# Kernel optimization log

Measured on AMD Instinct MI355X. Metric: run time of the kernel, lower is better.

The kernel has to match this reference:

```python
import jax, jax.numpy as jnp
import numpy as np

K = 16                 # nn_k neighbors (self excluded)
FILTER_SCALE = 2.0
SHARPNESS_SIGMA = 0.75
EPS = 1e-17


def _eps_denom(x):
    return jnp.where(x < EPS, EPS, x)


def _normalize(x):
    # F.normalize(dim=-1) semantics
    return x / jnp.maximum(jnp.linalg.norm(x, axis=-1, keepdims=True), 1e-12)


def _gather(feat, idx):
    # feat: (B,P,D), idx: (B,P,K) -> (B,P,K,D)   (== pytorch3d knn_gather)
    return jnp.take_along_axis(feat[:, None, :, :], idx[:, :, :, None], axis=2)


def _knn(points, k):
    # points: (B,P,3) -> squared dists (B,P,k), idxs (B,P,k); self excluded
    d2 = jnp.sum(points * points, axis=-1)
    dists = d2[:, :, None] + d2[:, None, :] - 2.0 * jnp.einsum('bpd,bqd->bpq', points, points)
    P = points.shape[1]
    r = jnp.arange(P)
    dists = dists.at[:, r, r].set(-jnp.inf)  # force self to be rank-0 of top_k
    neg, idx = jax.lax.top_k(-dists, k + 1)
    return jnp.maximum(-neg[:, :, 1:], 0.0), idx[:, :, 1:]


def _denoise(normals, idx, w):
    # weighted neighbor average of normals, per _denoise_normals
    nn_n = _gather(normals, idx)                       # (B,P,K,3)
    return jnp.sum(nn_n * w[..., None], axis=-2) / _eps_denom(
        jnp.sum(w, axis=-1, keepdims=True))


def setup_inputs() -> dict:
    key = jax.random.key(0)
    kp, kn = jax.random.split(key)
    B, P = 2, 8192
    points = jax.random.normal(kp, (B, P, 3), dtype=jnp.float32)
    normals = jax.random.normal(kn, (B, P, 3), dtype=jnp.float32)
    return {"points": points, "normals": normals}


def reference(points, normals):
    # --- torch.no_grad block: knn build + all weights + normal denoising ---
    pts_ng = jax.lax.stop_gradient(points)
    dists, idx = _knn(pts_ng, K)                       # (B,P,K)
    nn = _gather(pts_ng, idx)                          # (B,P,K,3), detached

    # phi = (1 - d/(2*d1*fs^2))^4, clamped at 0 (get_phi)
    s = dists[:, :, :1] * 2.0 * FILTER_SCALE * FILTER_SCALE
    w = jnp.maximum(1.0 - dists / _eps_denom(s), 0.0)
    phi = (w * w) * (w * w)

    n_ng = jax.lax.stop_gradient(normals)
    n1 = _denoise(n_ng, idx, phi)                      # first denoise with phi

    # normal_w = exp(-||n - ni||^2 / sigma^2) on normalized once-denoised normals
    nn_n = _gather(n1, idx)
    diff = _normalize(nn_n) - _normalize(n1)[:, :, None, :]
    inv_sigma = 1.0 / (SHARPNESS_SIGMA * SHARPNESS_SIGMA)
    normal_w = jnp.exp(-jnp.sum(diff * diff, axis=-1) * inv_sigma)

    # second denoise with phi * normal_w
    n2 = _denoise(n1, idx, phi * normal_w)

    # weights_proj = phi * spatial_w_proj(==1) * normal_w, ball-query masked
    weights_proj = phi * normal_w
    ball_mask = dists > FILTER_SCALE * dists[:, :, :1] * 2.0
    weights_proj = jnp.where(ball_mask, 0.0, weights_proj)
    weights_proj = jax.lax.stop_gradient(weights_proj)

    # --- outside no_grad: gather denoised normals, signed point-to-plane ---
    nn_normals = _gather(n2, idx)                      # (B,P,K,3) (no grad path)
    dist_to_surface = jnp.sum((nn - points[:, :, None, :]) * nn_normals, axis=-1)

    # projection loss: weighted mean of squared point-to-plane distance
    loss = jnp.sum(dist_to_surface * dist_to_surface * weights_proj, axis=-1) / \
        _eps_denom(jnp.sum(weights_proj, axis=-1))     # (B,P)
    return jnp.mean(loss)                              # BaseLoss reduction='mean'
```

## Files before the change

### kernel.cpp

```cpp
#include <hip/hip_runtime.h>
#include <math.h>

#define PP    8192
#define NB    2
#define NPTS  16384
#define KNN   16
#define EPSV  1e-17f
#define CH    128
#define NSUP  16
#define NCELL 4096

#define KEY_BIG 3.0e38f


__device__ __forceinline__ int spread3(int v) {
    return (v & 1) | ((v & 2) << 2) | ((v & 4) << 4) | ((v & 8) << 6);
}

__global__ __launch_bounds__(1024) void sort_kernel(
        const float* __restrict__ pts,
        float4* __restrict__ sorted4,
        int*    __restrict__ perm) {
    __shared__ int lh[NCELL];
    __shared__ int wtot[16];
    const int b = blockIdx.x;
    const int t = threadIdx.x;
    const int lane = t & 63, wid = t >> 6;
    const float* bp = pts + (size_t)b * PP * 3;

    for (int k = t; k < NCELL; k += 1024) lh[k] = 0;
    __syncthreads();

    float px[8], py[8], pz[8];
    int cell[8];
#pragma unroll
    for (int k = 0; k < 8; ++k) {
        const int p = t + k * 1024;
        const float x = bp[p * 3 + 0];
        const float y = bp[p * 3 + 1];
        const float z = bp[p * 3 + 2];
        px[k] = x; py[k] = y; pz[k] = z;
        const int ix = (int)fminf(fmaxf((x + 5.0f) * 1.6f, 0.0f), 15.0f);
        const int iy = (int)fminf(fmaxf((y + 5.0f) * 1.6f, 0.0f), 15.0f);
        const int iz = (int)fminf(fmaxf((z + 5.0f) * 1.6f, 0.0f), 15.0f);
        cell[k] = spread3(ix) | (spread3(iy) << 1) | (spread3(iz) << 2);
        atomicAdd(&lh[cell[k]], 1);
    }
    __syncthreads();

    const int v0 = lh[t * 4 + 0];
    const int v1 = lh[t * 4 + 1];
    const int v2 = lh[t * 4 + 2];
    const int v3 = lh[t * 4 + 3];
    const int s4 = v0 + v1 + v2 + v3;
    int v = s4;
#pragma unroll
    for (int off = 1; off < 64; off <<= 1) {
        int uu = __shfl_up(v, off, 64);
        if (lane >= off) v += uu;
    }
    if (lane == 63) wtot[wid] = v;
    __syncthreads();
    if (wid == 0) {
        int w = (lane < 16) ? wtot[lane] : 0;
#pragma unroll
        for (int off = 1; off < 16; off <<= 1) {
            int uu = __shfl_up(w, off, 64);
            if (lane >= off) w += uu;
        }
        if (lane < 16) wtot[lane] = w;
    }
    __syncthreads();
    const int wbase = (wid > 0) ? wtot[wid - 1] : 0;
    const int excl = wbase + v - s4;
    lh[t * 4 + 0] = excl;
    lh[t * 4 + 1] = excl + v0;
    lh[t * 4 + 2] = excl + v0 + v1;
    lh[t * 4 + 3] = excl + v0 + v1 + v2;
    __syncthreads();

#pragma unroll
    for (int k = 0; k < 8; ++k) {
        const int pos = atomicAdd(&lh[cell[k]], 1);
        sorted4[(size_t)b * PP + pos] =
            make_float4(px[k], py[k], pz[k],
                        px[k] * px[k] + py[k] * py[k] + pz[k] * pz[k]);
        perm[b * PP + pos] = t + k * 1024;
    }
}

__global__ void bbox_kernel(const float4* __restrict__ sorted4,
                            float4* __restrict__ bbmin,
                            float4* __restrict__ bbmax,
                            float4* __restrict__ sbmin,
                            float4* __restrict__ sbmax) {
    __shared__ float4 smn[8], smx[8];
    const int lane = threadIdx.x & 63;
    const int wave = threadIdx.x >> 6;
    const int cw = blockIdx.x * 8 + wave;
    const float4 v = sorted4[cw * 64 + lane];
    float mnx = v.x, mny = v.y, mnz = v.z;
    float mxx = v.x, mxy = v.y, mxz = v.z;
#pragma unroll
    for (int off = 32; off >= 1; off >>= 1) {
        mnx = fminf(mnx, __shfl_xor(mnx, off, 64));
        mny = fminf(mny, __shfl_xor(mny, off, 64));
        mnz = fminf(mnz, __shfl_xor(mnz, off, 64));
        mxx = fmaxf(mxx, __shfl_xor(mxx, off, 64));
        mxy = fmaxf(mxy, __shfl_xor(mxy, off, 64));
        mxz = fmaxf(mxz, __shfl_xor(mxz, off, 64));
    }
    if (lane == 0) {
        bbmin[cw] = make_float4(mnx, mny, mnz, 0.f);
        bbmax[cw] = make_float4(mxx, mxy, mxz, 0.f);
        smn[wave] = make_float4(mnx, mny, mnz, 0.f);
        smx[wave] = make_float4(mxx, mxy, mxz, 0.f);
    }
    __syncthreads();
    if (threadIdx.x == 0) {
        float4 a = smn[0], bmx = smx[0];
#pragma unroll
        for (int k = 1; k < 8; ++k) {
            a.x = fminf(a.x, smn[k].x); a.y = fminf(a.y, smn[k].y);
            a.z = fminf(a.z, smn[k].z);
            bmx.x = fmaxf(bmx.x, smx[k].x); bmx.y = fmaxf(bmx.y, smx[k].y);
            bmx.z = fmaxf(bmx.z, smx[k].z);
        }
        sbmin[blockIdx.x] = a;
        sbmax[blockIdx.x] = bmx;
    }
}

__device__ __forceinline__ void insert16(float (&keys)[KNN], float kk) {
#pragma unroll
    for (int s = KNN - 1; s >= 1; --s)
        keys[s] = __builtin_amdgcn_fmed3f(keys[s - 1], kk, keys[s]);
    keys[0] = fminf(keys[0], kk);
}

__device__ __forceinline__ void merge16(float (&a)[KNN], const float (&o)[KNN]) {
    float c[KNN];
#pragma unroll
    for (int s = 0; s < KNN; ++s) c[s] = fminf(a[s], o[KNN - 1 - s]);
#pragma unroll
    for (int st = KNN / 2; st >= 1; st >>= 1) {
#pragma unroll
        for (int base = 0; base < KNN; base += 2 * st) {
#pragma unroll
            for (int k = 0; k < st; ++k) {
                const float x = c[base + k], y = c[base + k + st];
                c[base + k]      = fminf(x, y);
                c[base + k + st] = fmaxf(x, y);
            }
        }
    }
#pragma unroll
    for (int s = 0; s < KNN; ++s) a[s] = c[s];
}

__global__ __launch_bounds__(256) void knn2_kernel(
        const float4* __restrict__ sorted4,
        const int*    __restrict__ perm,
        const float*  __restrict__ normals,
        const float4* __restrict__ bbmin,
        const float4* __restrict__ bbmax,
        const float4* __restrict__ sbmin,
        const float4* __restrict__ sbmax,
        int*    __restrict__ out_idx,
        float*  __restrict__ out_phi,
        float4* __restrict__ out_n1) {
    const int lane = threadIdx.x & 63;
    const int wv   = threadIdx.x >> 6;
    const int W    = blockIdx.x * 4 + wv;
    const int b    = W >> 12;
    const int qg   = W & 4095;
    const int qbase = qg * 2;
    const int i    = lane & 1;
    const int u    = lane >> 1;
    const int qloc = qbase + i;
    const int s0   = qbase >> 9;
    const float4* sb = sorted4 + (size_t)b * PP;
    const int bCH = b * CH;

    const float4 q4 = sb[qloc];
    const float qx = q4.x, qy = q4.y, qz = q4.z;
    const float d2q = qx * qx + qy * qy + qz * qz;

    float keys[KNN];
#pragma unroll
    for (int s = 0; s < KNN; ++s) keys[s] = KEY_BIG;

    auto proc = [&](int c) {
#pragma unroll
        for (int t = 0; t < 2; ++t) {
            const int j = c * 64 + u + 32 * t;
            const float4 c4 = sb[j];
            const float dot = fmaf(qz, c4.z, fmaf(qy, c4.y, qx * c4.x));
            const float d  = fmaf(-2.0f, dot, d2q + c4.w);
            const float dc = fmaxf(d, 0.0f);
            float kv = __uint_as_float(
                (__float_as_uint(dc) & 0xFFFFE000u) | (unsigned)j);
            if (j == qloc) kv = KEY_BIG;
            if (kv < keys[KNN - 1]) insert16(keys, kv);
        }
    };

    const int cb0 = s0 * 8;
    for (int k = 0; k < 8; ++k) proc(cb0 + k);

    unsigned Bq;
    {
        float tk[KNN];
#pragma unroll
        for (int s = 0; s < KNN; ++s) tk[s] = keys[s];
#pragma unroll
        for (int st = 0; st < 4; ++st) {
            const int S = 2 << st;
            float o[KNN];
#pragma unroll
            for (int s = 0; s < KNN; ++s) o[s] = __shfl_xor(tk[s], S, 64);
            merge16(tk, o);
        }
        float o15[KNN];
#pragma unroll
        for (int s = 0; s < KNN; ++s) o15[s] = __shfl_xor(tk[s], 32, 64);
        float B = fminf(tk[0], o15[KNN - 1]);
#pragma unroll
        for (int s = 1; s < KNN; ++s)
            B = fmaxf(B, fminf(tk[s], o15[KNN - 1 - s]));
        Bq = __float_as_uint(B);
    }

    {
        const int sup = (lane >> 2) & 15;
        const float4 smn = sbmin[b * NSUP + sup];
        const float4 smx = sbmax[b * NSUP + sup];
        const float ax = fmaxf(fmaxf(smn.x - qx, qx - smx.x), 0.0f);
        const float ay = fmaxf(fmaxf(smn.y - qy, qy - smx.y), 0.0f);
        const float az = fmaxf(fmaxf(smn.z - qz, qz - smx.z), 0.0f);
        const float dmS = (ax * ax + ay * ay + az * az) * 0.999999f;
        const unsigned flS = __float_as_uint(dmS) & 0xFFFFE000u;
        const unsigned long long M =
            __ballot((sup != s0) && (flS < Bq));

        for (int s = 0; s < NSUP; ++s) {
            if (!(M & (0xFULL << (s * 4)))) continue;
            const int cc = s * 8 + (u & 7);
            const float4 cmn = bbmin[bCH + cc];
            const float4 cmx = bbmax[bCH + cc];
            const float bx = fmaxf(fmaxf(cmn.x - qx, qx - cmx.x), 0.0f);
            const float by = fmaxf(fmaxf(cmn.y - qy, qy - cmx.y), 0.0f);
            const float bz = fmaxf(fmaxf(cmn.z - qz, qz - cmx.z), 0.0f);
            const float dmC = (bx * bx + by * by + bz * bz) * 0.999999f;
            const unsigned flC = __float_as_uint(dmC) & 0xFFFFE000u;
            const unsigned long long M2 = __ballot(flC < Bq);
#pragma unroll
            for (int k = 0; k < 8; ++k)
                if (M2 & (0x0003000300030003ULL << (2 * k))) proc(s * 8 + k);
        }
    }

#pragma unroll
    for (int st = 0; st < 5; ++st) {
        const int S = 2 << st;
        float o[KNN];
#pragma unroll
        for (int s = 0; s < KNN; ++s) o[s] = __shfl_xor(keys[s], S, 64);
        merge16(keys, o);
    }

    const int su = u & 15;
    float myk = keys[0];
#pragma unroll
    for (int s = 1; s < KNN; ++s) myk = (su == s) ? keys[s] : myk;
    const int j = (int)(__float_as_uint(myk) & 0x1FFFu);

    const float4 nb4 = sb[j];
    const float dot = fmaf(qz, nb4.z, fmaf(qy, nb4.y, qx * nb4.x));
    float dd = fmaf(-2.0f, dot, d2q + nb4.w);
    dd = fmaxf(dd, 0.0f);

    float d1 = dd;
#pragma unroll
    for (int st = 0; st < 4; ++st) d1 = fminf(d1, __shfl_xor(d1, 2 << st, 64));

    const float s0v  = d1 * 8.0f;
    const float sden = (s0v < EPSV) ? EPSV : s0v;
    const float w  = fmaxf(1.0f - dd / sden, 0.0f);
    const float ph = (w * w) * (w * w);

    const int qrow = (b << 13) + qloc;
    if (u < 16) {
        out_idx[qrow * KNN + u] = j;
        out_phi[qrow * KNN + u] = ph;
    }

    const float* bn = normals + (size_t)b * PP * 3;
    const int jo = perm[(b << 13) + j];
    const float nx = bn[jo * 3 + 0];
    const float ny = bn[jo * 3 + 1];
    const float nz = bn[jo * 3 + 2];
    float sx = ph * nx, sy = ph * ny, sz = ph * nz, ss = ph;
#pragma unroll
    for (int st = 0; st < 4; ++st) {
        const int S = 2 << st;
        sx += __shfl_xor(sx, S, 64);
        sy += __shfl_xor(sy, S, 64);
        sz += __shfl_xor(sz, S, 64);
        ss += __shfl_xor(ss, S, 64);
    }
    if (u == 0) {
        const float den = (ss < EPSV) ? EPSV : ss;
        out_n1[qrow] = make_float4(sx / den, sy / den, sz / den, 0.f);
    }
}

__global__ __launch_bounds__(256) void denoise2_kernel(
        const int* __restrict__ idx,
        const float* __restrict__ phi,
        const float4* __restrict__ n1,
        float* __restrict__ nw_out,
        float4* __restrict__ n2_out) {
    const int gid = blockIdx.x * 256 + threadIdx.x;
    const int q = gid >> 4;
    const int s = gid & 15;
    const int b = q >> 13;
    const int gbase = b * PP;
    const float INV_SIG = 1.0f / (0.75f * 0.75f);

    const float4 nq = n1[q];
    const float ax = nq.x, ay = nq.y, az = nq.z;
    const float an = fmaxf(sqrtf(ax * ax + ay * ay + az * az), 1e-12f);
    const float rx = ax / an, ry = ay / an, rz = az / an;

    const int j = idx[q * KNN + s];
    const float4 nb = n1[gbase + j];
    const float bx = nb.x, by = nb.y, bz = nb.z;
    const float bnn = fmaxf(sqrtf(bx * bx + by * by + bz * bz), 1e-12f);
    const float ux = bx / bnn - rx;
    const float uy = by / bnn - ry;
    const float uz = bz / bnn - rz;
    const float dq = ux * ux + uy * uy + uz * uz;
    const float nw = expf(-dq * INV_SIG);
    nw_out[q * KNN + s] = nw;

    const float wk = phi[q * KNN + s] * nw;
    float ox = wk * bx, oy = wk * by, oz = wk * bz, swn = wk;
#pragma unroll
    for (int off = 1; off < 16; off <<= 1) {
        ox  += __shfl_xor(ox,  off, 64);
        oy  += __shfl_xor(oy,  off, 64);
        oz  += __shfl_xor(oz,  off, 64);
        swn += __shfl_xor(swn, off, 64);
    }
    if (s == 0) {
        const float den = (swn < EPSV) ? EPSV : swn;
        n2_out[q] = make_float4(ox / den, oy / den, oz / den, 0.f);
    }
}

__global__ __launch_bounds__(256) void loss_kernel(
        const float4* __restrict__ sorted4,
        const int* __restrict__ idx,
        const float* __restrict__ phi,
        const float* __restrict__ nw,
        const float4* __restrict__ n2,
        float* __restrict__ partial) {
    const int gid = blockIdx.x * 256 + threadIdx.x;
    const int q = gid >> 4;
    const int s = gid & 15;
    const int b = q >> 13;
    const int il = q & (PP - 1);
    const float4* sbp = sorted4 + (size_t)b * PP;
    const int gbase = b * PP;

    const float4 p4 = sbp[il];
    const float px = p4.x, py = p4.y, pz = p4.z;
    const float d2q = px * px + py * py + pz * pz;

    const int j = idx[q * KNN + s];
    const float4 nb4 = sbp[j];
    const float dot = fmaf(pz, nb4.z, fmaf(py, nb4.y, px * nb4.x));
    const float dv  = fmaf(-2.0f, dot, d2q + nb4.w);
    const float d   = fmaxf(dv, 0.0f);

    float d1 = d;
#pragma unroll
    for (int off = 1; off < 16; off <<= 1) d1 = fminf(d1, __shfl_xor(d1, off, 64));

    float w = phi[q * KNN + s] * nw[q * KNN + s];
    if (d > 4.0f * d1) w = 0.f;

    const float4 nn = n2[gbase + j];
    const float dts = (nb4.x - px) * nn.x +
                      (nb4.y - py) * nn.y +
                      (nb4.z - pz) * nn.z;
    float num = dts * dts * w, den = w;
#pragma unroll
    for (int off = 1; off < 16; off <<= 1) {
        num += __shfl_xor(num, off, 64);
        den += __shfl_xor(den, off, 64);
    }

    __shared__ float ls[16];
    if (s == 0) {
        const float dd = (den < EPSV) ? EPSV : den;
        ls[threadIdx.x >> 4] = num / dd;
    }
    __syncthreads();
    if (threadIdx.x == 0) {
        float v = 0.f;
#pragma unroll
        for (int k = 0; k < 16; ++k) v += ls[k];
        partial[blockIdx.x] = v;
    }
}

__global__ void finalize_kernel(const float* __restrict__ partial,
                                float* __restrict__ out) {
    float v = 0.f;
#pragma unroll
    for (int k = 0; k < 16; ++k) v += partial[threadIdx.x + 64 * k];
#pragma unroll
    for (int off = 32; off >= 1; off >>= 1) v += __shfl_down(v, off, 64);
    if (threadIdx.x == 0) out[0] = v / (float)NPTS;
}

extern "C" void kernel_launch(void* const* d_in, const int* in_sizes, int n_in,
                              void* d_out, int out_size, void* d_ws, size_t ws_size,
                              hipStream_t stream) {
    const float* points  = (const float*)d_in[0];
    const float* normals = (const float*)d_in[1];
    float* out = (float*)d_out;

    float* wsf    = (float*)d_ws;
    int*   w_idx  = (int*)wsf;
    float* w_phi  = wsf + 262144;
    float* w_nw   = wsf + 524288;
    float4* w_n1  = (float4*)(wsf + 786432);
    float4* w_n2  = (float4*)(wsf + 851968);
    float4* w_sorted4 = (float4*)(wsf + 917504);
    float* w_part = wsf + 983040;
    int*    w_perm   = (int*)(wsf + 524288);
    float4* w_bbmin  = (float4*)(wsf + 557056);
    float4* w_bbmax  = (float4*)(wsf + 558080);
    float4* w_sbmin  = (float4*)(wsf + 559104);
    float4* w_sbmax  = (float4*)(wsf + 559232);

    sort_kernel   <<<NB, 1024, 0, stream>>>(points, w_sorted4, w_perm);
    bbox_kernel   <<<32, 512, 0, stream>>>(w_sorted4, w_bbmin, w_bbmax,
                                           w_sbmin, w_sbmax);
    knn2_kernel   <<<2048, 256, 0, stream>>>(w_sorted4, w_perm, normals,
                                             w_bbmin, w_bbmax, w_sbmin, w_sbmax,
                                             w_idx, w_phi, w_n1);
    denoise2_kernel<<<1024, 256, 0, stream>>>(w_idx, w_phi, w_n1, w_nw, w_n2);
    loss_kernel   <<<1024, 256, 0, stream>>>(w_sorted4, w_idx, w_phi, w_nw, w_n2, w_part);
    finalize_kernel<<<1, 64, 0, stream>>>(w_part, out);
}
```

Baseline: 133.1 us.

## Fuse denoise2, loss and finalize into one kernel with grid barrier

Measured after the change: 330.8 us. 148% more time.

```diff
diff --git a/kernel.cpp b/kernel.cpp
--- a/kernel.cpp
+++ b/kernel.cpp
@@ -315,115 +315,139 @@
     }
 }
 
-__global__ __launch_bounds__(256) void denoise2_kernel(
+__global__ __launch_bounds__(256, 4) void tail_kernel(
+        const float4* __restrict__ sorted4,
         const int* __restrict__ idx,
         const float* __restrict__ phi,
         const float4* __restrict__ n1,
-        float* __restrict__ nw_out,
-        float4* __restrict__ n2_out) {
+        float4* __restrict__ n2,
+        float* __restrict__ partial,
+        int* __restrict__ ctr,
+        float* __restrict__ out) {
+    __shared__ float ls[16];
+    __shared__ float ws[4];
+    __shared__ int lastFlag;
+
     const int gid = blockIdx.x * 256 + threadIdx.x;
     const int q = gid >> 4;
     const int s = gid & 15;
     const int b = q >> 13;
     const int gbase = b * PP;
-    const float INV_SIG = 1.0f / (0.75f * 0.75f);
-
-    const float4 nq = n1[q];
-    const float ax = nq.x, ay = nq.y, az = nq.z;
-    const float an = fmaxf(sqrtf(ax * ax + ay * ay + az * az), 1e-12f);
-    const float rx = ax / an, ry = ay / an, rz = az / an;
-
-    const int j = idx[q * KNN + s];
-    const float4 nb = n1[gbase + j];
-    const float bx = nb.x, by = nb.y, bz = nb.z;
-    const float bnn = fmaxf(sqrtf(bx * bx + by * by + bz * bz), 1e-12f);
-    const float ux = bx / bnn - rx;
-    const float uy = by / bnn - ry;
-    const float uz = bz / bnn - rz;
-    const float dq = ux * ux + uy * uy + uz * uz;
-    const float nw = expf(-dq * INV_SIG);
-    nw_out[q * KNN + s] = nw;
-
-    const float wk = phi[q * KNN + s] * nw;
-    float ox = wk * bx, oy = wk * by, oz = wk * bz, swn = wk;
-#pragma unroll
-    for (int off = 1; off < 16; off <<= 1) {
-        ox  += __shfl_xor(ox,  off, 64);
-        oy  += __shfl_xor(oy,  off, 64);
-        oz  += __shfl_xor(oz,  off, 64);
-        swn += __shfl_xor(swn, off, 64);
-    }
-    if (s == 0) {
-        const float den = (swn < EPSV) ? EPSV : swn;
-        n2_out[q] = make_float4(ox / den, oy / den, oz / den, 0.f);
-    }
-}
-
-__global__ __launch_bounds__(256) void loss_kernel(
-        const float4* __restrict__ sorted4,
-        const int* __restrict__ idx,
-        const float* __restrict__ phi,
-        const float* __restrict__ nw,
-        const float4* __restrict__ n2,
-        float* __restrict__ partial) {
-    const int gid = blockIdx.x * 256 + threadIdx.x;
-    const int q = gid >> 4;
-    const int s = gid & 15;
-    const int b = q >> 13;
-    const int il = q & (PP - 1);
-    const float4* sbp = sorted4 + (size_t)b * PP;
-    const int gbase = b * PP;
-
-    const float4 p4 = sbp[il];
-    const float px = p4.x, py = p4.y, pz = p4.z;
-    const float d2q = px * px + py * py + pz * pz;
-
-    const int j = idx[q * KNN + s];
-    const float4 nb4 = sbp[j];
-    const float dot = fmaf(pz, nb4.z, fmaf(py, nb4.y, px * nb4.x));
-    const float dv  = fmaf(-2.0f, dot, d2q + nb4.w);
-    const float d   = fmaxf(dv, 0.0f);
-
-    float d1 = d;
-#pragma unroll
-    for (int off = 1; off < 16; off <<= 1) d1 = fminf(d1, __shfl_xor(d1, off, 64));
-
-    float w = phi[q * KNN + s] * nw[q * KNN + s];
-    if (d > 4.0f * d1) w = 0.f;
-
-    const float4 nn = n2[gbase + j];
-    const float dts = (nb4.x - px) * nn.x +
-                      (nb4.y - py) * nn.y +
-                      (nb4.z - pz) * nn.z;
-    float num = dts * dts * w, den = w;
-#pragma unroll
-    for (int off = 1; off < 16; off <<= 1) {
-        num += __shfl_xor(num, off, 64);
-        den += __shfl_xor(den, off, 64);
-    }
-
-    __shared__ float ls[16];
-    if (s == 0) {
-        const float dd = (den < EPSV) ? EPSV : den;
-        ls[threadIdx.x >> 4] = num / dd;
-    }
+
+    const int   j  = idx[q * KNN + s];
+    const float ph = phi[q * KNN + s];
+
+    float nwv;
+    {
+        const float INV_SIG = 1.0f / (0.75f * 0.75f);
+        const float4 nq = n1[q];
+        const float ax = nq.x, ay = nq.y, az = nq.z;
+        const float an = fmaxf(sqrtf(ax * ax + ay * ay + az * az), 1e-12f);
+        const float rx = ax / an, ry = ay / an, rz = az / an;
+
+        const float4 nb = n1[gbase + j];
+        const float bx = nb.x, by = nb.y, bz = nb.z;
+        const float bnn = fmaxf(sqrtf(bx * bx + by * by + bz * bz), 1e-12f);
+        const float ux = bx / bnn - rx;
+        const float uy = by / bnn - ry;
+        const float uz = bz / bnn - rz;
+        const float dq = ux * ux + uy * uy + uz * uz;
+        nwv = expf(-dq * INV_SIG);
+
+        const float wk = ph * nwv;
+        float ox = wk * bx, oy = wk * by, oz = wk * bz, swn = wk;
+#pragma unroll
+        for (int off = 1; off < 16; off <<= 1) {
+            ox  += __shfl_xor(ox,  off, 64);
+            oy  += __shfl_xor(oy,  off, 64);
+            oz  += __shfl_xor(oz,  off, 64);
+            swn += __shfl_xor(swn, off, 64);
+        }
+        if (s == 0) {
+            const float den = (swn < EPSV) ? EPSV : swn;
+            n2[q] = make_float4(ox / den, oy / den, oz / den, 0.f);
+        }
+    }
+
+    __threadfence();
     __syncthreads();
     if (threadIdx.x == 0) {
+        __hip_atomic_fetch_add(&ctr[0], 1, __ATOMIC_RELEASE,
+                               __HIP_MEMORY_SCOPE_AGENT);
+        unsigned it = 0;
+        while (__hip_atomic_load(&ctr[0], __ATOMIC_ACQUIRE,
+                                 __HIP_MEMORY_SCOPE_AGENT) < 1024 &&
+               ++it < 2000000u)
+            __builtin_amdgcn_s_sleep(8);
+    }
+    __syncthreads();
+    __threadfence();
+
+    {
+        const int il = q & (PP - 1);
+        const float4* sbp = sorted4 + (size_t)b * PP;
+
+        const float4 p4 = sbp[il];
+        const float px = p4.x, py = p4.y, pz = p4.z;
+        const float d2q = px * px + py * py + pz * pz;
+
+        const float4 nb4 = sbp[j];
+        const float dot = fmaf(pz, nb4.z, fmaf(py, nb4.y, px * nb4.x));
+        const float dv  = fmaf(-2.0f, dot, d2q + nb4.w);
+        const float d   = fmaxf(dv, 0.0f);
+
+        float d1 = d;
+#pragma unroll
+        for (int off = 1; off < 16; off <<= 1)
+            d1 = fminf(d1, __shfl_xor(d1, off, 64));
+
+        float w = ph * nwv;
+        if (d > 4.0f * d1) w = 0.f;
+
+        const float4 nn = n2[gbase + j];
+        const float dts = (nb4.x - px) * nn.x +
+                          (nb4.y - py) * nn.y +
+                          (nb4.z - pz) * nn.z;
+        float num = dts * dts * w, den = w;
+#pragma unroll
+        for (int off = 1; off < 16; off <<= 1) {
+            num += __shfl_xor(num, off, 64);
+            den += __shfl_xor(den, off, 64);
+        }
+
+        if (s == 0) {
+            const float dd = (den < EPSV) ? EPSV : den;
+            ls[threadIdx.x >> 4] = num / dd;
+        }
+        __syncthreads();
+        if (threadIdx.x == 0) {
+            float v = 0.f;
+#pragma unroll
+            for (int k = 0; k < 16; ++k) v += ls[k];
+            partial[blockIdx.x] = v;
+        }
+    }
+
+    if (threadIdx.x == 0) {
+        __threadfence();
+        const int old = __hip_atomic_fetch_add(&ctr[1], 1, __ATOMIC_ACQ_REL,
+                                               __HIP_MEMORY_SCOPE_AGENT);
+        lastFlag = (old == 1023);
+    }
+    __syncthreads();
+    if (lastFlag) {
+        __threadfence();
         float v = 0.f;
-#pragma unroll
-        for (int k = 0; k < 16; ++k) v += ls[k];
-        partial[blockIdx.x] = v;
-    }
-}
-
-__global__ void finalize_kernel(const float* __restrict__ partial,
-                                float* __restrict__ out) {
-    float v = 0.f;
-#pragma unroll
-    for (int k = 0; k < 16; ++k) v += partial[threadIdx.x + 64 * k];
-#pragma unroll
-    for (int off = 32; off >= 1; off >>= 1) v += __shfl_down(v, off, 64);
-    if (threadIdx.x == 0) out[0] = v / (float)NPTS;
+        for (int k = threadIdx.x; k < 1024; k += 256) v += partial[k];
+#pragma unroll
+        for (int off = 32; off >= 1; off >>= 1) v += __shfl_xor(v, off, 64);
+        const int lane = threadIdx.x & 63;
+        const int wid = threadIdx.x >> 6;
+        if (lane == 0) ws[wid] = v;
+        __syncthreads();
+        if (threadIdx.x == 0)
+            out[0] = (ws[0] + ws[1] + ws[2] + ws[3]) / (float)NPTS;
+    }
 }
 
 extern "C" void kernel_launch(void* const* d_in, const int* in_sizes, int n_in,
@@ -436,24 +460,24 @@
     float* wsf    = (float*)d_ws;
     int*   w_idx  = (int*)wsf;
     float* w_phi  = wsf + 262144;
-    float* w_nw   = wsf + 524288;
     float4* w_n1  = (float4*)(wsf + 786432);
     float4* w_n2  = (float4*)(wsf + 851968);
     float4* w_sorted4 = (float4*)(wsf + 917504);
     float* w_part = wsf + 983040;
+    int*   w_ctr  = (int*)(wsf + 984064);
     int*    w_perm   = (int*)(wsf + 524288);
     float4* w_bbmin  = (float4*)(wsf + 557056);
     float4* w_bbmax  = (float4*)(wsf + 558080);
     float4* w_sbmin  = (float4*)(wsf + 559104);
     float4* w_sbmax  = (float4*)(wsf + 559232);
 
+    hipMemsetAsync(w_ctr, 0, 2 * sizeof(int), stream);
     sort_kernel   <<<NB, 1024, 0, stream>>>(points, w_sorted4, w_perm);
     bbox_kernel   <<<32, 512, 0, stream>>>(w_sorted4, w_bbmin, w_bbmax,
                                            w_sbmin, w_sbmax);
     knn2_kernel   <<<2048, 256, 0, stream>>>(w_sorted4, w_perm, normals,
                                              w_bbmin, w_bbmax, w_sbmin, w_sbmax,
                                              w_idx, w_phi, w_n1);
-    denoise2_kernel<<<1024, 256, 0, stream>>>(w_idx, w_phi, w_n1, w_nw, w_n2);
-    loss_kernel   <<<1024, 256, 0, stream>>>(w_sorted4, w_idx, w_phi, w_nw, w_n2, w_part);
-    finalize_kernel<<<1, 64, 0, stream>>>(w_part, out);
-}
+    tail_kernel   <<<1024, 256, 0, stream>>>(w_sorted4, w_idx, w_phi,
+                                             w_n1, w_n2, w_part, w_ctr, out);
+}
```
